# Kernel optimization log

Measured on AMD Instinct MI355X. Metric: run time of the kernel, lower is better.

Reference implementation:

```python
import jax, jax.numpy as jnp
import numpy as np
from jax import lax

H, W = 128, 128
K_JUNC = 300
STEPS = 32
THRESH = 0.008
BIAS_SPAN = 1
SCALE = 5.0
SENTINEL = K_JUNC * K_JUNC


def decode_hafm(angs, dist, bias):
    # angs [B,3,H,W], dist [B,1,H,W], bias [B,1,H,W] -> lines [B,3,H,W,4]
    bias_range = jnp.arange(-BIAS_SPAN, BIAS_SPAN + 1, dtype=jnp.float32).reshape(1, -1, 1, 1)
    d = jnp.clip(dist + bias * bias_range, 0.0, 1.0)  # [B,3,H,W]
    angle0 = (angs[:, 0:1] - 0.5) * jnp.pi * 2
    angle1 = angs[:, 1:2] * jnp.pi / 2
    angle2 = -angs[:, 2:3] * jnp.pi / 2
    c0, s0 = jnp.cos(angle0), jnp.sin(angle0)
    t1, t2 = jnp.tan(angle1), jnp.tan(angle2)
    x1 = (c0 - s0 * t1) * d * SCALE
    y1 = (s0 + c0 * t1) * d * SCALE
    x2 = (c0 - s0 * t2) * d * SCALE
    y2 = (s0 + c0 * t2) * d * SCALE
    y0, x0 = jnp.meshgrid(jnp.arange(H, dtype=jnp.float32), jnp.arange(W, dtype=jnp.float32), indexing='ij')
    x0 = x0[None, None]
    y0 = y0[None, None]
    x1 = jnp.clip(x1 + x0, 0, W - 1)
    y1 = jnp.clip(y1 + y0, 0, H - 1)
    x2 = jnp.clip(x2 + x0, 0, W - 1)
    y2 = jnp.clip(y2 + y0, 0, H - 1)
    return jnp.stack((x1, y1, x2, y2), axis=-1)


def propose_junctions(jloc, joff):
    # jloc [H,W], joff [2,H,W]; 3x3 NMS + top-K, thresholded junctions
    pooled = lax.reduce_window(jloc, -jnp.inf, lax.max, (3, 3), (1, 1), 'SAME')
    nms = jnp.where(jloc == pooled, jloc, 0.0)
    scores, idx = lax.top_k(nms.reshape(-1), K_JUNC)
    y = (idx // W).astype(jnp.float32)
    x = (idx % W).astype(jnp.float32)
    xs = x + joff[0].reshape(-1)[idx]
    ys = y + joff[1].reshape(-1)[idx]
    coords = jnp.stack([xs, ys], axis=-1)  # [K,2]
    valid = scores > THRESH
    coords = jnp.where(valid[:, None], coords, 1e6)
    return coords, scores


def bilinear_sample(fmap, px, py):
    # fmap [C,H,W]; px,py [N,S] -> [C,N,S]
    C = fmap.shape[0]
    px = jnp.clip(px, 0.0, W - 1)
    py = jnp.clip(py, 0.0, H - 1)
    x0 = jnp.floor(px)
    y0 = jnp.floor(py)
    x0i = x0.astype(jnp.int32)
    y0i = y0.astype(jnp.int32)
    x1i = jnp.minimum(x0i + 1, W - 1)
    y1i = jnp.minimum(y0i + 1, H - 1)
    wx = px - x0
    wy = py - y0
    flat = fmap.reshape(C, H * W)

    def g(yi, xi):
        return flat[:, (yi * W + xi).reshape(-1)].reshape(C, *px.shape)

    return (g(y0i, x0i) * (1 - wx) * (1 - wy)
            + g(y0i, x1i) * wx * (1 - wy)
            + g(y1i, x0i) * (1 - wx) * wy
            + g(y1i, x1i) * wx * wy)


def setup_inputs() -> dict:
    key = jax.random.key(0)
    ks = jax.random.split(key, 10)
    return {
        'features': jax.random.normal(ks[0], (1, 256, H, W), jnp.float32),
        'heatmaps': jax.random.normal(ks[1], (1, 9, H, W), jnp.float32),
        'fc1_w': jax.random.normal(ks[2], (128, 256), jnp.float32) * 0.05,
        'fc1_b': jax.random.normal(ks[3], (128,), jnp.float32) * 0.05,
        'w1': jax.random.normal(ks[4], (1024, 1024), jnp.float32) * 0.03,
        'b1': jnp.zeros((1024,), jnp.float32),
        'w2': jax.random.normal(ks[5], (1024, 1024), jnp.float32) * 0.03,
        'b2': jnp.zeros((1024,), jnp.float32),
        'w3': jax.random.normal(ks[6], (1, 1024), jnp.float32) * 0.03,
        'b3': jnp.zeros((1,), jnp.float32),
    }


def reference(features, heatmaps, fc1_w, fc1_b, w1, b1, w2, b2, w3, b3):
    angs = jax.nn.sigmoid(heatmaps[:, 0:3])
    dist = jax.nn.sigmoid(heatmaps[:, 3:4])
    bias = jax.nn.sigmoid(heatmaps[:, 4:5])
    jloc = jax.nn.softmax(heatmaps[:, 5:7], axis=1)[0, 1]  # [H,W]
    joff = jax.nn.sigmoid(heatmaps[0, 7:9])                # [2,H,W]

    junc, _ = propose_junctions(jloc, joff)                # [K,2]
    lines = decode_hafm(angs, dist, bias).reshape(-1, 4)   # [N,4], N=3*H*W
    N = lines.shape[0]

    # junction-to-endpoint matching (cdist + argmin)
    d1 = ((junc[:, None, :] - lines[None, :, :2]) ** 2).sum(-1)  # [K,N]
    d2 = ((junc[:, None, :] - lines[None, :, 2:]) ** 2).sum(-1)
    j1 = jnp.argmin(d1, axis=0)
    j2 = jnp.argmin(d2, axis=0)
    lo = jnp.minimum(j1, j2)
    hi = jnp.maximum(j1, j2)
    ids = jnp.where(lo < hi, lo * K_JUNC + hi, SENTINEL)
    # fixed-size dedup (masked analogue of torch unique(dim=0))
    uids = jnp.unique(ids, size=N, fill_value=SENTINEL)
    valid = uids < SENTINEL
    uids_safe = jnp.where(valid, uids, 0)
    p1 = junc[uids_safe // K_JUNC]
    p2 = junc[uids_safe % K_JUNC]
    line_coords = jnp.where(valid[:, None], jnp.concatenate([p1, p2], axis=-1), 0.0)  # [N,4]

    # LOI feature sampling
    loi = jnp.einsum('oc,chw->ohw', fc1_w, features[0]) + fc1_b[:, None, None]  # [128,H,W]
    t = jnp.linspace(0.0, 1.0, STEPS)[None, :]
    px = line_coords[:, 0:1] * t + line_coords[:, 2:3] * (1 - t)  # [N,32]
    py = line_coords[:, 1:2] * t + line_coords[:, 3:4] * (1 - t)
    feats = bilinear_sample(loi, px, py)            # [128,N,32]
    feats = feats.transpose(1, 0, 2)                # [N,128,32]
    feats = feats.reshape(N, 128, STEPS // 4, 4).max(-1)  # max_pool1d k=4
    feats = feats.reshape(N, 1024)

    h = jax.nn.relu(feats @ w1.T + b1)
    h = jax.nn.relu(h @ w2.T + b2)
    logits = (h @ w3.T + b3)[:, 0]
    line_scores = jax.nn.sigmoid(logits) * valid
    return line_coords, line_scores
```

## Files before the change

kernel.cpp:

```cpp
#include <hip/hip_runtime.h>
#include <math.h>

#define HH 128
#define WW 128
#define HW 16384
#define NLINES 49152
#define KJ 300
#define SENT 90000
#define THRESHV 0.008f
#define CAND_CAP 4096
#define BITWORDS 2816

typedef __attribute__((ext_vector_type(8))) short bf16x8;
typedef __attribute__((ext_vector_type(4))) float f32x4;

__device__ __forceinline__ float sigm(float x){ return 1.0f/(1.0f+expf(-x)); }

__device__ __forceinline__ short tobf(float f){
  unsigned u = __float_as_uint(f);
  unsigned r = u + 0x7FFFu + ((u >> 16) & 1u);
  return (short)(r >> 16);
}
__device__ __forceinline__ float bflo(unsigned u){ return __uint_as_float(u << 16); }
__device__ __forceinline__ float bfhi(unsigned u){ return __uint_as_float(u & 0xFFFF0000u); }

#define GLOAD_LDS16(g, l) \
  __builtin_amdgcn_global_load_lds((const __attribute__((address_space(1))) void*)(g), \
                                   (__attribute__((address_space(3))) void*)(l), 16, 0, 0)

__device__ __forceinline__ float jloc_at(const float* hm, int idx){
  float h5 = hm[5*HW + idx], h6 = hm[6*HW + idx];
  float mx = fmaxf(h5,h6);
  float e5 = expf(h5-mx), e6 = expf(h6-mx);
  return e6/(e5+e6);
}

__global__ __launch_bounds__(256) void k_front(const float* __restrict__ hm,
    const float* __restrict__ feat, const float* __restrict__ fc1w,
    float* __restrict__ lines, unsigned long long* __restrict__ cand,
    int* __restrict__ cand_count, short* __restrict__ featT, short* __restrict__ fc1b16,
    float* __restrict__ outZero){
  __shared__ float tile[32][33];
  __shared__ float jl[4][128];
  int b = blockIdx.x, t = threadIdx.x;
  if (b < 64){
    int i = b*256 + t;
    float h0 = hm[i], h1 = hm[HW+i], h2 = hm[2*HW+i], h3 = hm[3*HW+i], h4 = hm[4*HW+i];
    float a0 = sigm(h0), a1 = sigm(h1), a2 = sigm(h2);
    float dist = sigm(h3), bias = sigm(h4);
    const float PI = 3.14159265358979323846f;
    float ang0 = (a0-0.5f)*(2.0f*PI);
    float c0 = cosf(ang0), s0 = sinf(ang0);
    float t1 = tanf(a1*(0.5f*PI));
    float t2 = tanf(-a2*(0.5f*PI));
    int y = i >> 7, x = i & 127;
    float fx = (float)x, fy = (float)y;
    #pragma unroll
    for (int c=0;c<3;c++){
      float d = fminf(fmaxf(dist + bias*(float)(c-1), 0.0f), 1.0f);
      float ds = d*5.0f;
      float x1 = fminf(fmaxf((c0 - s0*t1)*ds + fx, 0.0f), 127.0f);
      float y1 = fminf(fmaxf((s0 + c0*t1)*ds + fy, 0.0f), 127.0f);
      float x2 = fminf(fmaxf((c0 - s0*t2)*ds + fx, 0.0f), 127.0f);
      float y2 = fminf(fmaxf((s0 + c0*t2)*ds + fy, 0.0f), 127.0f);
      ((float4*)lines)[c*HW + i] = make_float4(x1,y1,x2,y2);
    }
    int y0 = 2*b;
    #pragma unroll
    for (int idx = t; idx < 512; idx += 256){
      int r = idx >> 7, xx = idx & 127;
      int yy = y0 - 1 + r;
      jl[r][xx] = (yy >= 0 && yy < HH) ? jloc_at(hm, yy*WW + xx) : -1e30f;
    }
    __syncthreads();
    int lr = 1 + (t >> 7);
    float v = jl[lr][x];
    float m = v;
    #pragma unroll
    for (int dy=-1; dy<=1; dy++){
      #pragma unroll
      for (int dx=-1; dx<=1; dx++){
        int nx = x + dx; if (nx < 0 || nx >= WW) continue;
        m = fmaxf(m, jl[lr+dy][nx]);
      }
    }
    if (v == m && v > THRESHV){
      int pos = atomicAdd(cand_count, 1);
      if (pos < CAND_CAP){
        unsigned int vb = __float_as_uint(v);
        cand[pos] = ((unsigned long long)vb << 32) | (unsigned long long)(0xFFFFFFFFu - (unsigned)i);
      }
    }
  } else if (b < 64 + 4096){
    int idx = b - 64;
    int p0 = (idx & 511) * 32, c0 = (idx >> 9) * 32;
    int c  = t >> 3;
    int p4 = (t & 7) * 4;
    float4 v = *(const float4*)&feat[(size_t)(c0 + c)*HW + p0 + p4];
    tile[c][p4+0] = v.x; tile[c][p4+1] = v.y; tile[c][p4+2] = v.z; tile[c][p4+3] = v.w;
    __syncthreads();
    int p  = t >> 3;
    int cg = (t & 7) * 4;
    ushort4 o;
    o.x = (unsigned short)tobf(tile[cg+0][p]);
    o.y = (unsigned short)tobf(tile[cg+1][p]);
    o.z = (unsigned short)tobf(tile[cg+2][p]);
    o.w = (unsigned short)tobf(tile[cg+3][p]);
    *(ushort4*)&featT[(size_t)(p0 + p)*256 + c0 + cg] = o;
  } else if (b < 4288){
    int j = (b - 4160)*256 + t;
    fc1b16[j] = tobf(fc1w[j]);
  } else {
    int j = (b - 4288)*256 + t;
    ((float4*)outZero)[j] = make_float4(0.f,0.f,0.f,0.f);
  }
}

__global__ __launch_bounds__(1024) void k_mid(
    const unsigned long long* __restrict__ cand, const int* __restrict__ cand_count,
    const float* __restrict__ hm, float* __restrict__ junc,
    const short* __restrict__ featT, const short* __restrict__ fc1b16,
    const float* __restrict__ fc1b, short* __restrict__ loi){
  __shared__ __align__(16) char smem[CAND_CAP*8];
  __shared__ int wsum16[16];
  __shared__ int sBbin, sScnt;
  int b = blockIdx.x, t = threadIdx.x;
  if (b == 0){
    int* hist = (int*)smem;
    unsigned long long* sel = (unsigned long long*)(smem + 8192);
    unsigned long long* sfull = (unsigned long long*)smem;
    int count = *cand_count; if (count > CAND_CAP) count = CAND_CAP;
    int need = count < KJ ? count : KJ;
    hist[t] = 0; hist[t + 1024] = 0;
    if (t == 0){ sScnt = 0; sBbin = -1; }
    __syncthreads();
    for (int i=t; i<count; i+=1024){
      int bin = (int)(cand[i] >> 52) & 0x7FF;
      atomicAdd(&hist[bin], 1);
    }
    __syncthreads();
    int c0 = hist[2*t], c1 = hist[2*t+1];
    int pairv = c0 + c1;
    int v = pairv;
    #pragma unroll
    for (int d=1; d<64; d<<=1){
      int nv = __shfl_down(v, d, 64);
      if ((t & 63) + d < 64) v += nv;
    }
    if ((t & 63) == 0) wsum16[t >> 6] = v;
    __syncthreads();
    if (t < 16){
      int x = wsum16[t];
      #pragma unroll
      for (int d=1; d<16; d<<=1){
        int nv = __shfl_down(x, d, 16);
        if (t + d < 16) x += nv;
      }
      wsum16[t] = x;
    }
    __syncthreads();
    int w = t >> 6;
    int after = (w < 15) ? wsum16[w+1] : 0;
    int suf = v + after;
    int A_hi = suf - pairv;
    int A_lo = A_hi + c1;
    if (need > 0){
      if (A_hi < need && need <= A_hi + c1)      sBbin = 2*t+1;
      else if (A_lo < need && need <= A_lo + c0) sBbin = 2*t;
    }
    __syncthreads();
    int Bbin = sBbin;
    if (Bbin >= 0){
      for (int i=t; i<count; i+=1024){
        unsigned long long k = cand[i];
        int bin = (int)(k >> 52) & 0x7FF;
        if (bin >= Bbin){
          int p = atomicAdd(&sScnt, 1);
          if (p < 2048) sel[p] = k;
        }
      }
    }
    __syncthreads();
    int S = sScnt;
    bool fb = (S > 2048);
    if (!fb){
      int n2 = 512; while (n2 < S) n2 <<= 1;
      for (int i=t; i<n2; i+=1024) if (i >= S) sel[i] = 0ull;
      __syncthreads();
      for (int k=2; k<=n2; k<<=1){
        for (int j=k>>1; j>0; j>>=1){
          for (int i=t; i<n2; i+=1024){
            int ixj = i ^ j;
            if (ixj > i){
              unsigned long long a = sel[i], bb = sel[ixj];
              bool desc = ((i & k) == 0);
              if (desc ? (a < bb) : (a > bb)){ sel[i] = bb; sel[ixj] = a; }
            }
          }
          __syncthreads();
        }
      }
    } else {
      int n2 = 512; while (n2 < count) n2 <<= 1;
      __syncthreads();
      for (int i=t; i<n2; i+=1024) sfull[i] = (i < count) ? cand[i] : 0ull;
      __syncthreads();
      for (int k=2; k<=n2; k<<=1){
        for (int j=k>>1; j>0; j>>=1){
          for (int i=t; i<n2; i+=1024){
            int ixj = i ^ j;
            if (ixj > i){
              unsigned long long a = sfull[i], bb = sfull[ixj];
              bool desc = ((i & k) == 0);
              if (desc ? (a < bb) : (a > bb)){ sfull[i] = bb; sfull[ixj] = a; }
            }
          }
          __syncthreads();
        }
      }
    }
    if (t < KJ){
      float jxv = 1e6f, jyv = 1e6f;
      if (t < count){
        unsigned long long kk = fb ? sfull[t] : sel[t];
        unsigned idx = 0xFFFFFFFFu - (unsigned)(kk & 0xFFFFFFFFull);
        int yy = (int)(idx >> 7), xx = (int)(idx & 127u);
        jxv = (float)xx + sigm(hm[7*HW + idx]);
        jyv = (float)yy + sigm(hm[8*HW + idx]);
      }
      junc[2*t] = jxv; junc[2*t+1] = jyv;
    }
  } else {
    if (t >= 256) return;
    short* As = (short*)smem;
    short* Bs = (short*)(smem + 8192);
    int rb = (b - 1) * 64;
    int lane = t & 63, wave = t >> 6;
    int l16 = lane & 15, quad = lane >> 4;
    int srow = lane >> 3, schunk = (lane & 7) ^ srow;
    f32x4 acc[8];
    #pragma unroll
    for (int g=0; g<8; g++) acc[g] = (f32x4){0,0,0,0};
    for (int k0=0; k0<256; k0+=64){
      #pragma unroll
      for (int i=0; i<2; i++){
        int r0 = wave*16 + i*8;
        GLOAD_LDS16(featT + (size_t)(rb + r0 + srow)*256 + k0 + schunk*8, &As[r0*64]);
      }
      #pragma unroll
      for (int i=0; i<4; i++){
        int r0 = wave*32 + i*8;
        GLOAD_LDS16(fc1b16 + (size_t)(r0 + srow)*256 + k0 + schunk*8, &Bs[r0*64]);
      }
      __syncthreads();
      #pragma unroll
      for (int s2=0; s2<2; s2++){
        int slot = (s2*4 + quad) ^ (l16 & 7);
        bf16x8 a = *(const bf16x8*)&As[(wave*16 + l16)*64 + slot*8];
        #pragma unroll
        for (int g=0; g<8; g++){
          bf16x8 bv = *(const bf16x8*)&Bs[(g*16 + l16)*64 + slot*8];
          acc[g] = __builtin_amdgcn_mfma_f32_16x16x32_bf16(a, bv, acc[g], 0, 0, 0);
        }
      }
      __syncthreads();
    }
    int rowbase = rb + wave*16 + quad*4;
    #pragma unroll
    for (int g=0; g<8; g++){
      int col = g*16 + l16;
      float bs = fc1b[col];
      #pragma unroll
      for (int r=0; r<4; r++)
        loi[(size_t)(rowbase + r)*128 + col] = tobf(acc[g][r] + bs);
    }
  }
}

__global__ __launch_bounds__(256) void k_match(const float* __restrict__ lines,
    const float* __restrict__ junc, unsigned* __restrict__ bm,
    const float* __restrict__ w1, const float* __restrict__ w2,
    short* __restrict__ w1b, short* __restrict__ w2b){
  __shared__ float jx[KJ], jy[KJ];
  int b = blockIdx.x, t = threadIdx.x;
  if (b < 192){
    for (int k=t; k<KJ; k+=256){ jx[k] = junc[2*k]; jy[k] = junc[2*k+1]; }
    __syncthreads();
    int n = b*256 + t;
    float4 L = ((const float4*)lines)[n];
    float b1 = 1e30f, b2 = 1e30f; int j1 = 0, j2 = 0;
    #pragma unroll 4
    for (int k=0; k<KJ; k++){
      float dx1 = jx[k]-L.x, dy1 = jy[k]-L.y;
      float d1 = dx1*dx1 + dy1*dy1;
      float dx2 = jx[k]-L.z, dy2 = jy[k]-L.w;
      float d2 = dx2*dx2 + dy2*dy2;
      if (d1 < b1){ b1 = d1; j1 = k; }
      if (d2 < b2){ b2 = d2; j2 = k; }
    }
    int lo = min(j1,j2), hi = max(j1,j2);
    if (lo < hi){
      int id = lo*KJ + hi;
      atomicOr(&bm[id >> 5], 1u << (id & 31));
    }
  } else {
    int j = (b - 192)*256 + t;
    w1b[j] = tobf(w1[j]);
    w2b[j] = tobf(w2[j]);
  }
}

__global__ __launch_bounds__(1024) void k_unique(const unsigned* __restrict__ bm,
    int* __restrict__ uid_list, int* __restrict__ mcount){
  __shared__ int wsum[16];
  int t = threadIdx.x;
  int w0 = t*3;
  unsigned wv[3];
  int local = 0;
  #pragma unroll
  for (int i=0; i<3; i++){
    int w = w0 + i;
    wv[i] = (w < BITWORDS) ? bm[w] : 0u;
    local += __popc(wv[i]);
  }
  int v = local;
  #pragma unroll
  for (int d=1; d<64; d<<=1){
    int nv = __shfl_up(v, d, 64);
    if ((t & 63) >= d) v += nv;
  }
  if ((t & 63) == 63) wsum[t >> 6] = v;
  __syncthreads();
  if (t < 16){
    int x = wsum[t];
    #pragma unroll
    for (int d=1; d<16; d<<=1){
      int nv = __shfl_up(x, d, 16);
      if (t >= d) x += nv;
    }
    wsum[t] = x;
  }
  __syncthreads();
  int base = v - local + ((t >> 6) ? wsum[(t >> 6) - 1] : 0);
  #pragma unroll
  for (int i=0; i<3; i++){
    unsigned bits = wv[i];
    while (bits){
      int bb = __ffs(bits) - 1;
      uid_list[base++] = (w0 + i)*32 + bb;
      bits &= bits - 1;
    }
  }
  if (t == 1023) *mcount = wsum[15];
}

__global__ __launch_bounds__(256) void k_sample(float* __restrict__ out,
    const int* __restrict__ uid_list, const float* __restrict__ junc,
    const short* __restrict__ loi, const int* __restrict__ mcount,
    short* __restrict__ fbuf, float* __restrict__ logit, int chunk0, int chunk){
  __shared__ int4   sOffs[2][32];
  __shared__ float4 sWts[2][32];
  int M = *mcount;
  int t = threadIdx.x;
  int q  = t >> 6;
  int c2 = (t & 63) << 1;
  int lim = M - chunk0; if (lim > chunk) lim = chunk;
  for (int l0 = blockIdx.x*2; l0 < lim; l0 += gridDim.x*2){
    __syncthreads();
    if (t < 64){
      int pair = t >> 5, s = t & 31;
      int l = l0 + pair;
      if (l < lim){
        int r = chunk0 + l;
        int id = uid_list[r];
        int lo = id / KJ, hi = id % KJ;
        float2 P1 = ((const float2*)junc)[lo];
        float2 P2 = ((const float2*)junc)[hi];
        if (s == 0){
          ((float4*)out)[r] = make_float4(P1.x, P1.y, P2.x, P2.y);
          logit[l] = 0.0f;
        }
        float tt = (float)s * (1.0f/31.0f);
        float px = P1.x*tt + P2.x*(1.0f-tt);
        float py = P1.y*tt + P2.y*(1.0f-tt);
        px = fminf(fmaxf(px, 0.0f), 127.0f);
        py = fminf(fmaxf(py, 0.0f), 127.0f);
        float x0 = floorf(px), y0 = floorf(py);
        int x0i = (int)x0, y0i = (int)y0;
        int x1i = min(x0i+1, 127), y1i = min(y0i+1, 127);
        float wx = px - x0, wy = py - y0;
        sOffs[pair][s] = make_int4((y0i*WW + x0i)*128, (y0i*WW + x1i)*128,
                                   (y1i*WW + x0i)*128, (y1i*WW + x1i)*128);
        sWts[pair][s]  = make_float4((1.0f-wx)*(1.0f-wy), wx*(1.0f-wy),
                                     (1.0f-wx)*wy,        wx*wy);
      }
    }
    __syncthreads();
    #pragma unroll
    for (int pair=0; pair<2; pair++){
      int l = l0 + pair;
      if (l >= lim) break;
      float gl0=-1e30f, gl1=-1e30f, gh0=-1e30f, gh1=-1e30f;
      #pragma unroll
      for (int j=0; j<8; j++){
        int s = q*8 + j;
        int4 o   = sOffs[pair][s];
        float4 w = sWts[pair][s];
        unsigned u00 = *(const unsigned*)&loi[o.x + c2];
        unsigned u01 = *(const unsigned*)&loi[o.y + c2];
        unsigned u10 = *(const unsigned*)&loi[o.z + c2];
        unsigned u11 = *(const unsigned*)&loi[o.w + c2];
        float vlo = w.x*bflo(u00) + w.y*bflo(u01) + w.z*bflo(u10) + w.w*bflo(u11);
        float vhi = w.x*bfhi(u00) + w.y*bfhi(u01) + w.z*bfhi(u10) + w.w*bfhi(u11);
        if (j < 4){ gl0 = fmaxf(gl0, vlo); gh0 = fmaxf(gh0, vhi); }
        else      { gl1 = fmaxf(gl1, vlo); gh1 = fmaxf(gh1, vhi); }
      }
      unsigned plo = ((unsigned)(unsigned short)tobf(gl0)) | (((unsigned)(unsigned short)tobf(gl1)) << 16);
      unsigned phi = ((unsigned)(unsigned short)tobf(gh0)) | (((unsigned)(unsigned short)tobf(gh1)) << 16);
      *(unsigned*)&fbuf[(size_t)l*1024 + c2*8 + q*2]     = plo;
      *(unsigned*)&fbuf[(size_t)l*1024 + (c2+1)*8 + q*2] = phi;
    }
  }
}

template<int MODE>
__global__ __launch_bounds__(256) void k_mlp(const short* __restrict__ A,
    const short* __restrict__ B, const float* __restrict__ bias,
    short* __restrict__ Hout, const float* __restrict__ w3,
    float* __restrict__ logit, const int* __restrict__ mcount, int chunk0){
  int M = *mcount;
  int rb = blockIdx.x * 64;
  if (chunk0 + rb >= M) return;
  int cb = blockIdx.y * 128;
  __shared__ short As[64*64];
  __shared__ short Bs[128*64];
  int lane = threadIdx.x & 63, wave = threadIdx.x >> 6;
  int l16 = lane & 15, quad = lane >> 4;
  int srow = lane >> 3, schunk = (lane & 7) ^ srow;
  f32x4 acc[8];
  #pragma unroll
  for (int g=0; g<8; g++) acc[g] = (f32x4){0,0,0,0};
  for (int k0=0; k0<1024; k0+=64){
    #pragma unroll
    for (int i=0; i<2; i++){
      int r0 = wave*16 + i*8;
      GLOAD_LDS16(A + (size_t)(rb + r0 + srow)*1024 + k0 + schunk*8, &As[r0*64]);
    }
    #pragma unroll
    for (int i=0; i<4; i++){
      int r0 = wave*32 + i*8;
      GLOAD_LDS16(B + (size_t)(cb + r0 + srow)*1024 + k0 + schunk*8, &Bs[r0*64]);
    }
    __syncthreads();
    #pragma unroll
    for (int s=0; s<2; s++){
      int slot = (s*4 + quad) ^ (l16 & 7);
      bf16x8 a = *(const bf16x8*)&As[(wave*16 + l16)*64 + slot*8];
      #pragma unroll
      for (int g=0; g<8; g++){
        bf16x8 bv = *(const bf16x8*)&Bs[(g*16 + l16)*64 + slot*8];
        acc[g] = __builtin_amdgcn_mfma_f32_16x16x32_bf16(a, bv, acc[g], 0, 0, 0);
      }
    }
    __syncthreads();
  }
  int rowbase = rb + wave*16 + quad*4;
  if (MODE == 0){
    #pragma unroll
    for (int g=0; g<8; g++){
      int col = cb + g*16 + l16;
      float bs = bias[col];
      #pragma unroll
      for (int r=0; r<4; r++)
        Hout[(size_t)(rowbase + r)*1024 + col] = tobf(fmaxf(acc[g][r] + bs, 0.0f));
    }
  } else {
    float p0[4] = {0,0,0,0};
    #pragma unroll
    for (int g=0; g<8; g++){
      int col = cb + g*16 + l16;
      float bs = bias[col], wv = w3[col];
      #pragma unroll
      for (int r=0; r<4; r++)
        p0[r] += fmaxf(acc[g][r] + bs, 0.0f) * wv;
    }
    #pragma unroll
    for (int r=0; r<4; r++){
      #pragma unroll
      for (int m=1; m<16; m<<=1)
        p0[r] += __shfl_xor(p0[r], m, 16);
    }
    if (l16 == 0){
      #pragma unroll
      for (int r=0; r<4; r++)
        atomicAdd(&logit[rowbase + r], p0[r]);
    }
  }
}

__global__ void k_score(const float* __restrict__ logit, const float* __restrict__ b3,
                        const int* __restrict__ mcount, float* __restrict__ out, int chunk0){
  int i = blockIdx.x*blockDim.x + threadIdx.x;
  int r = chunk0 + i;
  int M = *mcount;
  if (r >= M) return;
  float lg = logit[i] + b3[0];
  out[4*NLINES + r] = 1.0f/(1.0f + expf(-lg));
}

extern "C" void kernel_launch(void* const* d_in, const int* in_sizes, int n_in,
                              void* d_out, int out_size, void* d_ws, size_t ws_size,
                              hipStream_t stream){
  const float* features = (const float*)d_in[0];
  const float* heatmaps = (const float*)d_in[1];
  const float* fc1_w    = (const float*)d_in[2];
  const float* fc1_b    = (const float*)d_in[3];
  const float* w1       = (const float*)d_in[4];
  const float* b1       = (const float*)d_in[5];
  const float* w2       = (const float*)d_in[6];
  const float* b2       = (const float*)d_in[7];
  const float* w3       = (const float*)d_in[8];
  const float* b3       = (const float*)d_in[9];
  float* out = (float*)d_out;

  char* ws = (char*)d_ws;
  size_t off = 0;
  auto alloc = [&](size_t bytes) -> void* {
    void* p = ws + off;
    off = (off + bytes + 255) & ~(size_t)255;
    return p;
  };
  float* lines     = (float*)alloc((size_t)NLINES*16);
  unsigned long long* cand = (unsigned long long*)alloc(CAND_CAP*8);
  int*      cand_count = (int*)alloc(4);
  unsigned* bitmap     = (unsigned*)alloc(BITWORDS*4);
  size_t zlen = (size_t)((char*)(bitmap + BITWORDS) - (char*)cand_count);
  float* junc      = (float*)alloc(KJ*2*4);
  int*   uid_list  = (int*)alloc((size_t)45056*4);
  int*   mcount    = (int*)alloc(4);
  short* loi       = (short*)alloc((size_t)HW*128*2);
  short* featT     = (short*)alloc((size_t)HW*256*2);
  short* fc1b16    = (short*)alloc((size_t)128*256*2);
  short* w1b       = (short*)alloc((size_t)1024*1024*2);
  short* w2b       = (short*)alloc((size_t)1024*1024*2);
  size_t fixed = off;

  const int chunk_opts[4] = {45056, 22528, 11264, 5632};
  int CHUNK = 5632;
  for (int ci=0; ci<4; ci++){
    size_t need = fixed + (size_t)chunk_opts[ci]*1024*2*2 + (size_t)chunk_opts[ci]*4 + 1024;
    if (need <= ws_size){ CHUNK = chunk_opts[ci]; break; }
  }
  short* fbuf  = (short*)alloc((size_t)CHUNK*1024*2);
  short* h1buf = (short*)alloc((size_t)CHUNK*1024*2);
  float* logit = (float*)alloc((size_t)CHUNK*4);

  hipMemsetAsync(cand_count, 0, zlen, stream);
  k_front<<<4528, 256, 0, stream>>>(heatmaps, features, fc1_w, lines, cand,
                                    cand_count, featT, fc1b16, out);
  k_mid  <<<257, 1024, 0, stream>>>(cand, cand_count, heatmaps, junc, featT,
                                    fc1b16, fc1_b, loi);
  k_match<<<4288, 256, 0, stream>>>(lines, junc, bitmap, w1, w2, w1b, w2b);
  k_unique<<<1, 1024, 0, stream>>>(bitmap, uid_list, mcount);

  int nchunk = (45056 + CHUNK - 1) / CHUNK;
  for (int ci=0; ci<nchunk; ci++){
    int chunk0 = ci * CHUNK;
    k_sample<<<1024, 256, 0, stream>>>(out, uid_list, junc, loi, mcount, fbuf,
                                       logit, chunk0, CHUNK);
    dim3 g1(CHUNK/64, 8);
    k_mlp<0><<<g1, 256, 0, stream>>>(fbuf, w1b, b1, h1buf, nullptr,
                                     nullptr, mcount, chunk0);
    k_mlp<2><<<g1, 256, 0, stream>>>(h1buf, w2b, b2, nullptr, w3,
                                     logit, mcount, chunk0);
    k_score<<<(CHUNK+255)/256, 256, 0, stream>>>(logit, b3, mcount, out, chunk0);
  }
}
```

Before: 180.9 us.

## Switch MLP GEMM to 32x32x16 MFMA with 128x64 block tiles

```diff
diff --git a/kernel.cpp b/kernel.cpp
--- a/kernel.cpp
+++ b/kernel.cpp
@@ -13,6 +13,7 @@
 
 typedef __attribute__((ext_vector_type(8))) short bf16x8;
 typedef __attribute__((ext_vector_type(4))) float f32x4;
+typedef __attribute__((ext_vector_type(16))) float f32x16;
 
 __device__ __forceinline__ float sigm(float x){ return 1.0f/(1.0f+expf(-x)); }
 
@@ -429,71 +430,70 @@
     short* __restrict__ Hout, const float* __restrict__ w3,
     float* __restrict__ logit, const int* __restrict__ mcount, int chunk0){
   int M = *mcount;
-  int rb = blockIdx.x * 64;
+  int rb = blockIdx.x * 128;
   if (chunk0 + rb >= M) return;
-  int cb = blockIdx.y * 128;
-  __shared__ short As[64*64];
-  __shared__ short Bs[128*64];
+  int cb = blockIdx.y * 64;
+  __shared__ short As[128*64];
+  __shared__ short Bs[64*64];
   int lane = threadIdx.x & 63, wave = threadIdx.x >> 6;
-  int l16 = lane & 15, quad = lane >> 4;
+  int l32 = lane & 31, kg = lane >> 5;
   int srow = lane >> 3, schunk = (lane & 7) ^ srow;
-  f32x4 acc[8];
+  f32x16 acc0, acc1;
   #pragma unroll
-  for (int g=0; g<8; g++) acc[g] = (f32x4){0,0,0,0};
+  for (int i=0; i<16; i++){ acc0[i] = 0.0f; acc1[i] = 0.0f; }
   for (int k0=0; k0<1024; k0+=64){
+    #pragma unroll
+    for (int i=0; i<4; i++){
+      int r0 = wave*32 + i*8;
+      GLOAD_LDS16(A + (size_t)(rb + r0 + srow)*1024 + k0 + schunk*8, &As[r0*64]);
+    }
     #pragma unroll
     for (int i=0; i<2; i++){
       int r0 = wave*16 + i*8;
-      GLOAD_LDS16(A + (size_t)(rb + r0 + srow)*1024 + k0 + schunk*8, &As[r0*64]);
-    }
-    #pragma unroll
-    for (int i=0; i<4; i++){
-      int r0 = wave*32 + i*8;
       GLOAD_LDS16(B + (size_t)(cb + r0 + srow)*1024 + k0 + schunk*8, &Bs[r0*64]);
     }
     __syncthreads();
-    #pragma unroll
-    for (int s=0; s<2; s++){
-      int slot = (s*4 + quad) ^ (l16 & 7);
-      bf16x8 a = *(const bf16x8*)&As[(wave*16 + l16)*64 + slot*8];
-      #pragma unroll
-      for (int g=0; g<8; g++){
-        bf16x8 bv = *(const bf16x8*)&Bs[(g*16 + l16)*64 + slot*8];
-        acc[g] = __builtin_amdgcn_mfma_f32_16x16x32_bf16(a, bv, acc[g], 0, 0, 0);
-      }
-    }
-    __syncthreads();
-  }
-  int rowbase = rb + wave*16 + quad*4;
+    int arow = wave*32 + l32;
+    #pragma unroll
+    for (int ks=0; ks<4; ks++){
+      int ck = ks*2 + kg;
+      bf16x8 a  = *(const bf16x8*)&As[arow*64 + (ck ^ (arow & 7))*8];
+      bf16x8 b0 = *(const bf16x8*)&Bs[l32*64      + (ck ^ (l32 & 7))*8];
+      bf16x8 b1 = *(const bf16x8*)&Bs[(32+l32)*64 + (ck ^ (l32 & 7))*8];
+      acc0 = __builtin_amdgcn_mfma_f32_32x32x16_bf16(a, b0, acc0, 0, 0, 0);
+      acc1 = __builtin_amdgcn_mfma_f32_32x32x16_bf16(a, b1, acc1, 0, 0, 0);
+    }
+    __syncthreads();
+  }
+  int rbase = rb + wave*32 + 4*kg;
   if (MODE == 0){
     #pragma unroll
-    for (int g=0; g<8; g++){
-      int col = cb + g*16 + l16;
-      float bs = bias[col];
-      #pragma unroll
-      for (int r=0; r<4; r++)
-        Hout[(size_t)(rowbase + r)*1024 + col] = tobf(fmaxf(acc[g][r] + bs, 0.0f));
+    for (int reg=0; reg<16; reg++){
+      int row = rbase + (reg&3) + 8*(reg>>2);
+      int col0 = cb + l32;
+      Hout[(size_t)row*1024 + col0]      = tobf(fmaxf(acc0[reg] + bias[col0],      0.0f));
+      Hout[(size_t)row*1024 + col0 + 32] = tobf(fmaxf(acc1[reg] + bias[col0 + 32], 0.0f));
     }
   } else {
-    float p0[4] = {0,0,0,0};
-    #pragma unroll
-    for (int g=0; g<8; g++){
-      int col = cb + g*16 + l16;
-      float bs = bias[col], wv = w3[col];
-      #pragma unroll
-      for (int r=0; r<4; r++)
-        p0[r] += fmaxf(acc[g][r] + bs, 0.0f) * wv;
-    }
-    #pragma unroll
-    for (int r=0; r<4; r++){
-      #pragma unroll
-      for (int m=1; m<16; m<<=1)
-        p0[r] += __shfl_xor(p0[r], m, 16);
-    }
-    if (l16 == 0){
-      #pragma unroll
-      for (int r=0; r<4; r++)
-        atomicAdd(&logit[rowbase + r], p0[r]);
+    int col0 = cb + l32;
+    float bs0 = bias[col0], wv0 = w3[col0];
+    float bs1 = bias[col0 + 32], wv1 = w3[col0 + 32];
+    float p[16];
+    #pragma unroll
+    for (int reg=0; reg<16; reg++){
+      p[reg] = fmaxf(acc0[reg] + bs0, 0.0f) * wv0
+             + fmaxf(acc1[reg] + bs1, 0.0f) * wv1;
+    }
+    #pragma unroll
+    for (int reg=0; reg<16; reg++){
+      #pragma unroll
+      for (int m=1; m<32; m<<=1)
+        p[reg] += __shfl_xor(p[reg], m, 32);
+    }
+    if (l32 == 0){
+      #pragma unroll
+      for (int reg=0; reg<16; reg++)
+        atomicAdd(&logit[rbase + (reg&3) + 8*(reg>>2)], p[reg]);
     }
   }
 }
@@ -568,7 +568,7 @@
     int chunk0 = ci * CHUNK;
     k_sample<<<1024, 256, 0, stream>>>(out, uid_list, junc, loi, mcount, fbuf,
                                        logit, chunk0, CHUNK);
-    dim3 g1(CHUNK/64, 8);
+    dim3 g1((CHUNK + 127)/128, 16);
     k_mlp<0><<<g1, 256, 0, stream>>>(fbuf, w1b, b1, h1buf, nullptr,
                                      nullptr, mcount, chunk0);
     k_mlp<2><<<g1, 256, 0, stream>>>(h1buf, w2b, b2, nullptr, w3,
```

Result: slower. 190.9 us (+5.5%).
